# Optimization experiments

Hardware: AMD Instinct MI355X
Metric: run time of the kernel (lower is better)

Reference implementation:

```python
import jax, jax.numpy as jnp
import numpy as np

D = 128      # d_feat / d_model
L = 512      # seq_len
H = 8        # heads (hardcoded in FourierBlock weights)
E = D // H   # head dim = 16
MODES = 64   # low-frequency modes (mode_select='low' -> index = range(MODES))
MA = 25      # moving_avg kernel
NL = 2       # e_layers
DFF = 512
EPS = 1e-5


def _positional(length, dim):
    pos = jnp.arange(length, dtype=jnp.float32)[:, None]
    div = jnp.exp(jnp.arange(0, dim, 2, dtype=jnp.float32) * (-np.log(10000.0) / dim))
    pe = jnp.zeros((length, dim), dtype=jnp.float32)
    pe = pe.at[:, 0::2].set(jnp.sin(pos * div))
    pe = pe.at[:, 1::2].set(jnp.cos(pos * div))
    return pe


def _mov_mean(x, k):
    # series_decomp moving average: replicate-pad (k-1)//2 each side, window mean stride 1
    pad = (k - 1) // 2
    xp = jnp.concatenate([jnp.repeat(x[:, :1], pad, axis=1), x,
                          jnp.repeat(x[:, -1:], pad, axis=1)], axis=1)
    cs = jnp.cumsum(xp, axis=1)
    cs = jnp.concatenate([jnp.zeros_like(cs[:, :1]), cs], axis=1)
    return (cs[:, k:] - cs[:, :-k]) / k


def _fourier_layer(x, Wq, bq, Wo, bo, fwr, fwi):
    # AutoCorrelationLayer(query proj -> FourierBlock -> out proj); k/v projections are unused by FourierBlock
    B = x.shape[0]
    q = (x @ Wq + bq).reshape(B, L, H, E).transpose(0, 2, 3, 1)   # B,H,E,L
    xft = jnp.fft.rfft(q, axis=-1)                                # B,H,E,L//2+1
    Wc = fwr + 1j * fwi                                           # H,E,E,M (complex mode weights)
    sel = jnp.einsum('bhem,heom->bhom', xft[..., :MODES], Wc)
    out_ft = jnp.zeros((B, H, E, L // 2 + 1), dtype=sel.dtype).at[..., :MODES].set(sel)
    y = jnp.fft.irfft(out_ft, n=L, axis=-1)                       # B,H,E,L
    y = y.reshape(B, L, H * E)  # matches torch .view(B, L, -1) on contiguous B,H,E,L
    return y @ Wo + bo


def _enc_layer(x, Wq, bq, Wo, bo, fwr, fwi, W1, W2):
    x = x + _fourier_layer(x, Wq, bq, Wo, bo, fwr, fwi)
    x = x - _mov_mean(x, MA)                                  # decomp1 seasonal part
    y = jax.nn.gelu(x @ W1, approximate=False) @ W2           # 1x1 convs == matmuls, no bias
    s = x + y
    return s - _mov_mean(s, MA)                               # decomp2 seasonal part


def setup_inputs() -> dict:
    key = jax.random.key(0)
    ks = jax.random.split(key, 12)
    B = 128
    scale = 1.0 / (D * D)
    return {
        "x_enc": jax.random.normal(ks[0], (B, D * L), dtype=jnp.float32),
        "x_mark_enc": jax.random.uniform(ks[1], (B, D * L), dtype=jnp.float32),
        "x_dec": jnp.zeros((1,), jnp.float32),
        "x_mark_dec": jnp.zeros((1,), jnp.float32),
        "conv_w": jax.random.normal(ks[2], (D, D, 3), dtype=jnp.float32) * 0.02,
        "Wq": jax.random.normal(ks[3], (NL, D, D), dtype=jnp.float32) * 0.02,
        "bq": jnp.zeros((NL, D), jnp.float32),
        "Wo": jax.random.normal(ks[4], (NL, D, D), dtype=jnp.float32) * 0.02,
        "bo": jnp.zeros((NL, D), jnp.float32),
        "fwr": jax.random.uniform(ks[5], (NL, H, E, E, MODES), dtype=jnp.float32) * scale,
        "fwi": jax.random.uniform(ks[6], (NL, H, E, E, MODES), dtype=jnp.float32) * scale,
        "W1": jax.random.normal(ks[7], (NL, D, DFF), dtype=jnp.float32) * 0.02,
        "W2": jax.random.normal(ks[8], (NL, DFF, D), dtype=jnp.float32) * 0.02,
        "ln_g": jnp.ones((D,), jnp.float32),
        "ln_b": jnp.zeros((D,), jnp.float32),
        "proj_w": jax.random.normal(ks[9], (D * L,), dtype=jnp.float32) * 0.002,
        "proj_b": jnp.zeros((), jnp.float32),
    }


def reference(x_enc, x_mark_enc, x_dec, x_mark_dec, conv_w, Wq, bq, Wo, bo,
              fwr, fwi, W1, W2, ln_g, ln_b, proj_w, proj_b):
    B = x_enc.shape[0]
    x = x_enc.reshape(B, D, L).transpose(0, 2, 1)          # B,L,D
    mark = x_mark_enc.reshape(B, D, L).transpose(0, 2, 1)  # B,L,D
    # TokenEmbedding: Conv1d kernel 3, circular padding, no bias
    xc = x.transpose(0, 2, 1)                              # B,D,L
    xp = jnp.concatenate([xc[:, :, -1:], xc, xc[:, :, :1]], axis=-1)
    tok = jax.lax.conv_general_dilated(xp, conv_w, (1,), 'VALID',
                                       dimension_numbers=('NCH', 'OIH', 'NCH'))
    h = tok.transpose(0, 2, 1) + _positional(L, D)[None]   # + sinusoidal PE (dropout=0)
    for l in range(NL):
        h = _enc_layer(h, Wq[l], bq[l], Wo[l], bo[l], fwr[l], fwi[l], W1[l], W2[l])
    # my_Layernorm: LayerNorm over features, then subtract mean over time axis
    mu = h.mean(-1, keepdims=True)
    var = h.var(-1, keepdims=True)
    hn = (h - mu) / jnp.sqrt(var + EPS) * ln_g + ln_b
    hn = hn - hn.mean(axis=1, keepdims=True)
    o = jax.nn.gelu(hn, approximate=False) * mark          # act + mask-mul
    return o.reshape(B, -1) @ proj_w + proj_b              # (B,) after squeeze
```

## Files before the change

kernel.cpp:

```cpp
#include <hip/hip_runtime.h>
#include <math.h>

#define DFF 512
#define NLAYER 2
#define CS_LD 130
#define SS_LD 130
#define TS2_LD 68

typedef __bf16 bf16x8 __attribute__((ext_vector_type(8)));
typedef __bf16 bf16x4 __attribute__((ext_vector_type(4)));
typedef float f32x4 __attribute__((ext_vector_type(4)));

__device__ __forceinline__ float4 f4_load(const float* p) { return *(const float4*)p; }
__device__ __forceinline__ void f4_store(float* p, float4 v) { *(float4*)p = v; }
__device__ __forceinline__ float4 f4_zero() { return make_float4(0.f, 0.f, 0.f, 0.f); }
__device__ __forceinline__ float gelu_f(float x) {
    return 0.5f * x * (1.0f + erff(x * 0.70710678118654752440f));
}
__device__ __forceinline__ float gelu_fast(float x) {
    float z = 1.5957691216f * (x + 0.044715f * x * x * x);
    float e = __expf(z);
    return x - x / (e + 1.0f);
}
__device__ __forceinline__ void store_bf4(__bf16* p, float4 v) {
    __bf16 t[4] = {(__bf16)v.x, (__bf16)v.y, (__bf16)v.z, (__bf16)v.w};
    *(uint2*)p = *(uint2*)t;
}
__device__ __forceinline__ bf16x8 ld_b64x2(const __bf16* p) {
    bf16x4 lo = *(const bf16x4*)p;
    bf16x4 hi = *(const bf16x4*)(p + 4);
    return __builtin_shufflevector(lo, hi, 0, 1, 2, 3, 4, 5, 6, 7);
}
__device__ __forceinline__ int clampl(int v) { return v < 0 ? 0 : (v > 511 ? 511 : v); }

__global__ __launch_bounds__(256) void k_init(float* __restrict__ pe,
                                              __bf16* __restrict__ Fttb,
                                              __bf16* __restrict__ Gtb) {
    int idx = blockIdx.x * 256 + threadIdx.x;
    {
        int l = idx >> 7, d = idx & 127;
        int j = d >> 1;
        double div = exp((double)(2 * j) * (-log(10000.0) / 128.0));
        double a = (double)l * div;
        pe[idx] = (d & 1) ? (float)cos(a) : (float)sin(a);
    }
    {
        int m2 = idx >> 9, t = idx & 511;
        int m = m2 >> 1;
        int r = (m * t) & 511;
        double ang = (double)r * (6.283185307179586476925287 / 512.0);
        float cv = (float)cos(ang), sv = (float)sin(ang);
        float f = (m2 & 1) ? -sv : cv;
        Fttb[idx] = (__bf16)f;
        float s = (m == 0) ? (1.0f / 512.0f) : (2.0f / 512.0f);
        Gtb[t * 128 + m2] = (__bf16)(f * s);
    }
}

__global__ __launch_bounds__(256) void k_castw(const float* __restrict__ Wq,
                                               const float* __restrict__ Wo,
                                               const float* __restrict__ W1,
                                               const float* __restrict__ W2,
                                               const float* __restrict__ cw,
                                               __bf16* __restrict__ wbf,
                                               __bf16* __restrict__ cwtk) {
    int i = blockIdx.x * 256 + threadIdx.x;
    if (i < 65536) {
        int r = i & 16383, l = (i >> 14) & 1;
        int n = r >> 7, k = r & 127;
        const float* W = (i >= 32768) ? Wo : Wq;
        wbf[i] = (__bf16)W[l * 16384 + k * 128 + n];
    } else if (i < 196608) {
        int j = i - 65536;
        int l = j >> 16, r = j & 65535;
        int f = r >> 7, k = r & 127;
        wbf[i] = (__bf16)W1[l * 65536 + k * 512 + f];
    } else if (i < 327680) {
        int j = i - 196608;
        int l = j >> 16, r = j & 65535;
        int n = r >> 9, f = r & 511;
        wbf[i] = (__bf16)W2[l * 65536 + f * 128 + n];
    } else if (i < 376832) {
        int j = i - 327680;
        int s = j >> 14, r = j & 16383;
        int d = r >> 7, ii = r & 127;
        cwtk[j] = (__bf16)cw[(d * 128 + ii) * 3 + s];
    }
}

__global__ __launch_bounds__(256) void k_xpose(const float* __restrict__ xe,
                                               __bf16* __restrict__ xt) {
    __shared__ float ts[128][65];
    const int b = blockIdx.y, l0 = blockIdx.x * 64;
    for (int idx = threadIdx.x; idx < 128 * 16; idx += 256) {
        int d = idx >> 4, c4 = idx & 15;
        float4 v = f4_load(&xe[((size_t)b * 128 + d) * 512 + l0 + c4 * 4]);
        ts[d][c4 * 4 + 0] = v.x; ts[d][c4 * 4 + 1] = v.y;
        ts[d][c4 * 4 + 2] = v.z; ts[d][c4 * 4 + 3] = v.w;
    }
    __syncthreads();
#pragma unroll
    for (int p = 0; p < 4; ++p) {
        int l = (threadIdx.x >> 4) + p * 16;
        int d0 = (threadIdx.x & 15) * 8;
        __bf16 tmp[8];
#pragma unroll
        for (int j = 0; j < 8; ++j) tmp[j] = (__bf16)ts[d0 + j][l];
        *(uint4*)&xt[((size_t)b * 512 + l0 + l) * 128 + d0] = *(uint4*)tmp;
    }
}

__global__ __launch_bounds__(256, 4) void k_embed_m(const __bf16* __restrict__ xt,
                                                    const __bf16* __restrict__ cwtk,
                                                    const float* __restrict__ pe,
                                                    float* __restrict__ h,
                                                    __bf16* __restrict__ hb) {
    const int b = blockIdx.x >> 3, l0 = (blockIdx.x & 7) * 64;
    const int lane = threadIdx.x & 63, wid = threadIdx.x >> 6;
    const int wrow = (wid & 1) * 32, wcol = (wid >> 1) * 64;
    const int m16 = lane & 15, quad = lane >> 4;
    f32x4 acc[2][4];
#pragma unroll
    for (int a = 0; a < 2; ++a)
#pragma unroll
        for (int bb = 0; bb < 4; ++bb) acc[a][bb] = {0.f, 0.f, 0.f, 0.f};
#pragma unroll
    for (int s = 0; s < 3; ++s) {
#pragma unroll
        for (int ks = 0; ks < 4; ++ks) {
            const int ko = ks * 32 + quad * 8;
            bf16x8 af[2], bfr[4];
#pragma unroll
            for (int rt = 0; rt < 2; ++rt) {
                int gl = (l0 + wrow + rt * 16 + m16 + s - 1) & 511;
                af[rt] = *(const bf16x8*)&xt[(((size_t)b * 512 + gl) << 7) + ko];
            }
#pragma unroll
            for (int ct = 0; ct < 4; ++ct)
                bfr[ct] = *(const bf16x8*)&cwtk[((size_t)(s * 128 + wcol + ct * 16 + m16) << 7) + ko];
#pragma unroll
            for (int rt = 0; rt < 2; ++rt)
#pragma unroll
                for (int ct = 0; ct < 4; ++ct)
                    acc[rt][ct] = __builtin_amdgcn_mfma_f32_16x16x32_bf16(
                        af[rt], bfr[ct], acc[rt][ct], 0, 0, 0);
        }
    }
#pragma unroll
    for (int ct = 0; ct < 4; ++ct) {
        int gcol = wcol + ct * 16 + m16;
#pragma unroll
        for (int rt = 0; rt < 2; ++rt)
#pragma unroll
            for (int r = 0; r < 4; ++r) {
                int l = l0 + wrow + rt * 16 + quad * 4 + r;
                float v = acc[rt][ct][r] + pe[l * 128 + gcol];
                size_t gi = (((size_t)b * 512 + l) << 7) + gcol;
                h[gi] = v;
                hb[gi] = (__bf16)v;
            }
    }
}

__global__ __launch_bounds__(256, 4) void k_qprojT(const __bf16* __restrict__ Xb,
                                                   const __bf16* __restrict__ Wt,
                                                   const float* __restrict__ bias,
                                                   __bf16* __restrict__ qT) {
    const int rowBase = blockIdx.x * 64;
    const int lane = threadIdx.x & 63, wid = threadIdx.x >> 6;
    const int wn = (wid & 1) * 64, wr = (wid >> 1) * 32;
    const int m16 = lane & 15, quad = lane >> 4;
    f32x4 acc[4][2];
#pragma unroll
    for (int a = 0; a < 4; ++a)
#pragma unroll
        for (int b = 0; b < 2; ++b) acc[a][b] = {0.f, 0.f, 0.f, 0.f};
#pragma unroll
    for (int ks = 0; ks < 4; ++ks) {
        const int ko = ks * 32 + quad * 8;
        bf16x8 wf[4], xf[2];
#pragma unroll
        for (int rt = 0; rt < 4; ++rt)
            wf[rt] = *(const bf16x8*)&Wt[((size_t)(wn + rt * 16 + m16) << 7) + ko];
#pragma unroll
        for (int ct = 0; ct < 2; ++ct)
            xf[ct] = *(const bf16x8*)&Xb[((size_t)(rowBase + wr + ct * 16 + m16) << 7) + ko];
#pragma unroll
        for (int rt = 0; rt < 4; ++rt)
#pragma unroll
            for (int ct = 0; ct < 2; ++ct)
                acc[rt][ct] = __builtin_amdgcn_mfma_f32_16x16x32_bf16(
                    wf[rt], xf[ct], acc[rt][ct], 0, 0, 0);
    }
#pragma unroll
    for (int rt = 0; rt < 4; ++rt)
#pragma unroll
        for (int r = 0; r < 4; ++r) {
            int n = wn + rt * 16 + quad * 4 + r;
            float bv = bias[n];
#pragma unroll
            for (int ct = 0; ct < 2; ++ct) {
                int grow = rowBase + wr + ct * 16 + m16;
                qT[(size_t)n * 65536 + grow] = (__bf16)(acc[rt][ct][r] + bv);
            }
        }
}

__global__ __launch_bounds__(128) void k_fdftmix(const __bf16* __restrict__ qT,
                                                 const __bf16* __restrict__ Fttb,
                                                 const float* __restrict__ fwr,
                                                 const float* __restrict__ fwi,
                                                 __bf16* __restrict__ ddb) {
    __shared__ float cs[32][CS_LD];
    const int b = blockIdx.y, d0 = blockIdx.x * 32;
    const int lane = threadIdx.x & 63, wid = threadIdx.x >> 6;
    const int wm = wid * 64;
    const int m16 = lane & 15, quad = lane >> 4;
    f32x4 acc[2][4];
#pragma unroll
    for (int a = 0; a < 2; ++a)
#pragma unroll
        for (int bb = 0; bb < 4; ++bb) acc[a][bb] = {0.f, 0.f, 0.f, 0.f};
    for (int ks = 0; ks < 16; ++ks) {
        const int ko = ks * 32 + quad * 8;
        bf16x8 af[2], bf[4];
#pragma unroll
        for (int rt = 0; rt < 2; ++rt)
            af[rt] = *(const bf16x8*)&qT[(size_t)(d0 + rt * 16 + m16) * 65536 + b * 512 + ko];
#pragma unroll
        for (int ct = 0; ct < 4; ++ct)
            bf[ct] = *(const bf16x8*)&Fttb[(size_t)(wm + ct * 16 + m16) * 512 + ko];
#pragma unroll
        for (int rt = 0; rt < 2; ++rt)
#pragma unroll
            for (int ct = 0; ct < 4; ++ct)
                acc[rt][ct] = __builtin_amdgcn_mfma_f32_16x16x32_bf16(
                    af[rt], bf[ct], acc[rt][ct], 0, 0, 0);
    }
#pragma unroll
    for (int rt = 0; rt < 2; ++rt)
#pragma unroll
        for (int ct = 0; ct < 4; ++ct)
#pragma unroll
            for (int r = 0; r < 4; ++r)
                cs[rt * 16 + quad * 4 + r][wm + ct * 16 + m16] = acc[rt][ct][r];
    __syncthreads();
    const int m = threadIdx.x & 63, og = threadIdx.x >> 6;
#pragma unroll
    for (int lh = 0; lh < 2; ++lh) {
        int hh = (d0 >> 4) + lh;
#pragma unroll
        for (int oi = 0; oi < 8; ++oi) {
            int o = og * 8 + oi;
            float dr = 0.f, di = 0.f;
#pragma unroll
            for (int e = 0; e < 16; ++e) {
                float2 cv = *(const float2*)&cs[lh * 16 + e][2 * m];
                float wr = fwr[(((size_t)hh * 16 + e) * 16 + o) * 64 + m];
                float wi = fwi[(((size_t)hh * 16 + e) * 16 + o) * 64 + m];
                dr += cv.x * wr - cv.y * wi;
                di += cv.x * wi + cv.y * wr;
            }
            __bf16 t2[2] = {(__bf16)dr, (__bf16)di};
            *(uint*)&ddb[((size_t)b * 128 + hh * 16 + o) * 128 + 2 * m] = *(uint*)t2;
        }
    }
}

__global__ __launch_bounds__(256, 4) void k_idft_m(const __bf16* __restrict__ ddb,
                                                   const __bf16* __restrict__ Gtb,
                                                   __bf16* __restrict__ y) {
    const int b = blockIdx.y;
    const int t0 = (blockIdx.x & 3) * 128, hob = (blockIdx.x >> 2) * 64;
    const int lane = threadIdx.x & 63, wid = threadIdx.x >> 6;
    const int wt = (wid & 1) * 64, wh = (wid >> 1) * 32;
    const int m16 = lane & 15, quad = lane >> 4;
    f32x4 acc[4][2];
#pragma unroll
    for (int a = 0; a < 4; ++a)
#pragma unroll
        for (int bb = 0; bb < 2; ++bb) acc[a][bb] = {0.f, 0.f, 0.f, 0.f};
#pragma unroll
    for (int ks = 0; ks < 4; ++ks) {
        const int ko = ks * 32 + quad * 8;
        bf16x8 af[4], bf[2];
#pragma unroll
        for (int rt = 0; rt < 4; ++rt)
            af[rt] = *(const bf16x8*)&Gtb[(size_t)(t0 + wt + rt * 16 + m16) * 128 + ko];
#pragma unroll
        for (int ct = 0; ct < 2; ++ct)
            bf[ct] = *(const bf16x8*)&ddb[((size_t)b * 128 + hob + wh + ct * 16 + m16) * 128 + ko];
#pragma unroll
        for (int rt = 0; rt < 4; ++rt)
#pragma unroll
            for (int ct = 0; ct < 2; ++ct)
                acc[rt][ct] = __builtin_amdgcn_mfma_f32_16x16x32_bf16(
                    af[rt], bf[ct], acc[rt][ct], 0, 0, 0);
    }
#pragma unroll
    for (int rt = 0; rt < 4; ++rt)
#pragma unroll
        for (int ct = 0; ct < 2; ++ct) {
            int ho = hob + wh + ct * 16 + m16;
            int tb = t0 + wt + rt * 16 + quad * 4;
            __bf16 tmp[4] = {(__bf16)acc[rt][ct][0], (__bf16)acc[rt][ct][1],
                             (__bf16)acc[rt][ct][2], (__bf16)acc[rt][ct][3]};
            *(uint2*)&y[((size_t)b * 128 + ho) * 512 + tb] = *(uint2*)tmp;
        }
}

__global__ __launch_bounds__(256, 3) void k_mgd(const __bf16* __restrict__ yb,
                                                const __bf16* __restrict__ Wt,
                                                const float* __restrict__ bias,
                                                const float* __restrict__ hres,
                                                float* __restrict__ outf,
                                                __bf16* __restrict__ outb) {
    __shared__ float ss[96 * SS_LD];
    const int b = blockIdx.x >> 3, l0 = (blockIdx.x & 7) * 64;
    const int lane = threadIdx.x & 63, wid = threadIdx.x >> 6;
    const int wrow = (wid & 1) * 48, wcol = (wid >> 1) * 64;
    const int m16 = lane & 15, quad = lane >> 4;
    f32x4 acc[3][4];
#pragma unroll
    for (int a = 0; a < 3; ++a)
#pragma unroll
        for (int bb = 0; bb < 4; ++bb) acc[a][bb] = {0.f, 0.f, 0.f, 0.f};
#pragma unroll
    for (int ks = 0; ks < 4; ++ks) {
        const int ko = ks * 32 + quad * 8;
        bf16x8 af[3], bfr[4];
#pragma unroll
        for (int rt = 0; rt < 3; ++rt) {
            int gl = clampl(l0 - 16 + wrow + rt * 16 + m16);
            af[rt] = *(const bf16x8*)&yb[(((size_t)b * 512 + gl) << 7) + ko];
        }
#pragma unroll
        for (int ct = 0; ct < 4; ++ct)
            bfr[ct] = *(const bf16x8*)&Wt[((size_t)(wcol + ct * 16 + m16) << 7) + ko];
#pragma unroll
        for (int rt = 0; rt < 3; ++rt)
#pragma unroll
            for (int ct = 0; ct < 4; ++ct)
                acc[rt][ct] = __builtin_amdgcn_mfma_f32_16x16x32_bf16(
                    af[rt], bfr[ct], acc[rt][ct], 0, 0, 0);
    }
#pragma unroll
    for (int ct = 0; ct < 4; ++ct) {
        int col = wcol + ct * 16 + m16;
        float bv = bias[col];
#pragma unroll
        for (int rt = 0; rt < 3; ++rt)
#pragma unroll
            for (int r = 0; r < 4; ++r) {
                int row = wrow + rt * 16 + quad * 4 + r;
                int gl = clampl(l0 - 16 + row);
                ss[row * SS_LD + col] =
                    acc[rt][ct][r] + bv + hres[(((size_t)b * 512 + gl) << 7) + col];
            }
    }
    __syncthreads();
    const int dg = threadIdx.x & 31, lg = threadIdx.x >> 5;
    const int d0 = dg * 4, base = lg * 8;
    float4 s = f4_zero();
#pragma unroll
    for (int w = 0; w < 25; ++w) {
        float4 v = f4_load(&ss[(base + 4 + w) * SS_LD + d0]);
        s.x += v.x; s.y += v.y; s.z += v.z; s.w += v.w;
    }
    const float inv = 1.0f / 25.0f;
#pragma unroll
    for (int i = 0; i < 8; ++i) {
        float4 x = f4_load(&ss[(base + 16 + i) * SS_LD + d0]);
        float4 o = make_float4(x.x - s.x * inv, x.y - s.y * inv,
                               x.z - s.z * inv, x.w - s.w * inv);
        size_t gi = (((size_t)b * 512 + l0 + base + i) << 7) + d0;
        f4_store(&outf[gi], o);
        store_bf4(&outb[gi], o);
        if (i < 7) {
            float4 a = f4_load(&ss[(base + 29 + i) * SS_LD + d0]);
            float4 r = f4_load(&ss[(base + 4 + i) * SS_LD + d0]);
            s.x += a.x - r.x; s.y += a.y - r.y; s.z += a.z - r.z; s.w += a.w - r.w;
        }
    }
}

__global__ __launch_bounds__(256, 3) void k_ffd(const __bf16* __restrict__ Xb,
                                                const float* __restrict__ Xf,
                                                const __bf16* __restrict__ W1t,
                                                const __bf16* __restrict__ W2t,
                                                float* __restrict__ outf,
                                                __bf16* __restrict__ outb) {
    __shared__ __align__(16) float ss[96 * SS_LD];
    __bf16* ts = (__bf16*)ss;
    const int b = blockIdx.x >> 3, l0 = (blockIdx.x & 7) * 64;
    const int lane = threadIdx.x & 63, wid = threadIdx.x >> 6;
    const int wrow = (wid & 1) * 48;
    const int wcolF = (wid >> 1) * 32;
    const int wcolO = (wid >> 1) * 64;
    const int m16 = lane & 15, quad = lane >> 4;
    f32x4 acc2[3][4];
#pragma unroll
    for (int a = 0; a < 3; ++a)
#pragma unroll
        for (int bb = 0; bb < 4; ++bb) acc2[a][bb] = {0.f, 0.f, 0.f, 0.f};

    for (int fc = 0; fc < 8; ++fc) {
        const int f0 = fc * 64;
        f32x4 c1[3][2];
#pragma unroll
        for (int a = 0; a < 3; ++a)
#pragma unroll
            for (int bb = 0; bb < 2; ++bb) c1[a][bb] = {0.f, 0.f, 0.f, 0.f};
#pragma unroll
        for (int ks = 0; ks < 4; ++ks) {
            const int ko = ks * 32 + quad * 8;
            bf16x8 af[3], bfr[2];
#pragma unroll
            for (int rt = 0; rt < 3; ++rt) {
                int gl = clampl(l0 - 16 + wrow + rt * 16 + m16);
                af[rt] = *(const bf16x8*)&Xb[(((size_t)b * 512 + gl) << 7) + ko];
            }
#pragma unroll
            for (int ct = 0; ct < 2; ++ct)
                bfr[ct] = *(const bf16x8*)&W1t[((size_t)(f0 + wcolF + ct * 16 + m16) << 7) + ko];
#pragma unroll
            for (int rt = 0; rt < 3; ++rt)
#pragma unroll
                for (int ct = 0; ct < 2; ++ct)
                    c1[rt][ct] = __builtin_amdgcn_mfma_f32_16x16x32_bf16(
                        af[rt], bfr[ct], c1[rt][ct], 0, 0, 0);
        }
#pragma unroll
        for (int rt = 0; rt < 3; ++rt)
#pragma unroll
            for (int ct = 0; ct < 2; ++ct)
#pragma unroll
                for (int r = 0; r < 4; ++r) {
                    int lrow = wrow + rt * 16 + quad * 4 + r;
                    int lcol = wcolF + ct * 16 + m16;
                    ts[lrow * TS2_LD + lcol] = (__bf16)gelu_fast(c1[rt][ct][r]);
                }
        __syncthreads();
#pragma unroll
        for (int ks2 = 0; ks2 < 2; ++ks2) {
            const int ko2 = ks2 * 32 + quad * 8;
            bf16x8 af[3], bfr[4];
#pragma unroll
            for (int rt = 0; rt < 3; ++rt)
                af[rt] = ld_b64x2(&ts[(wrow + rt * 16 + m16) * TS2_LD + ko2]);
#pragma unroll
            for (int ct = 0; ct < 4; ++ct)
                bfr[ct] = *(const bf16x8*)&W2t[((size_t)(wcolO + ct * 16 + m16) << 9) + f0 + ko2];
#pragma unroll
            for (int rt = 0; rt < 3; ++rt)
#pragma unroll
                for (int ct = 0; ct < 4; ++ct)
                    acc2[rt][ct] = __builtin_amdgcn_mfma_f32_16x16x32_bf16(
                        af[rt], bfr[ct], acc2[rt][ct], 0, 0, 0);
        }
        __syncthreads();
    }
#pragma unroll
    for (int ct = 0; ct < 4; ++ct) {
        int col = wcolO + ct * 16 + m16;
#pragma unroll
        for (int rt = 0; rt < 3; ++rt)
#pragma unroll
            for (int r = 0; r < 4; ++r) {
                int row = wrow + rt * 16 + quad * 4 + r;
                int gl = clampl(l0 - 16 + row);
                ss[row * SS_LD + col] =
                    acc2[rt][ct][r] + Xf[(((size_t)b * 512 + gl) << 7) + col];
            }
    }
    __syncthreads();
    const int dg = threadIdx.x & 31, lg = threadIdx.x >> 5;
    const int d0 = dg * 4, base = lg * 8;
    float4 s = f4_zero();
#pragma unroll
    for (int w = 0; w < 25; ++w) {
        float4 v = f4_load(&ss[(base + 4 + w) * SS_LD + d0]);
        s.x += v.x; s.y += v.y; s.z += v.z; s.w += v.w;
    }
    const float inv = 1.0f / 25.0f;
#pragma unroll
    for (int i = 0; i < 8; ++i) {
        float4 x = f4_load(&ss[(base + 16 + i) * SS_LD + d0]);
        float4 o = make_float4(x.x - s.x * inv, x.y - s.y * inv,
                               x.z - s.z * inv, x.w - s.w * inv);
        size_t gi = (((size_t)b * 512 + l0 + base + i) << 7) + d0;
        f4_store(&outf[gi], o);
        store_bf4(&outb[gi], o);
        if (i < 7) {
            float4 a = f4_load(&ss[(base + 29 + i) * SS_LD + d0]);
            float4 r = f4_load(&ss[(base + 4 + i) * SS_LD + d0]);
            s.x += a.x - r.x; s.y += a.y - r.y; s.z += a.z - r.z; s.w += a.w - r.w;
        }
    }
}

__global__ __launch_bounds__(256) void k_ln(const float* __restrict__ X,
                                            const float* __restrict__ g,
                                            const float* __restrict__ bb,
                                            float* __restrict__ out) {
    const int row = blockIdx.x * 4 + (threadIdx.x >> 6);
    const int lane = threadIdx.x & 63;
    float2 v = *(const float2*)&X[(size_t)row * 128 + lane * 2];
    float s = v.x + v.y, ss = v.x * v.x + v.y * v.y;
#pragma unroll
    for (int o = 32; o; o >>= 1) {
        s += __shfl_xor(s, o);
        ss += __shfl_xor(ss, o);
    }
    float mu = s * (1.0f / 128.0f);
    float var = ss * (1.0f / 128.0f) - mu * mu;
    float rstd = rsqrtf(var + 1e-5f);
    float2 gg = *(const float2*)&g[lane * 2];
    float2 bv = *(const float2*)&bb[lane * 2];
    float2 o;
    o.x = (v.x - mu) * rstd * gg.x + bv.x;
    o.y = (v.y - mu) * rstd * gg.y + bv.y;
    *(float2*)&out[(size_t)row * 128 + lane * 2] = o;
}

__global__ __launch_bounds__(128) void k_colmean(const float* __restrict__ X,
                                                 float* __restrict__ cm) {
    const int b = blockIdx.y, l0 = blockIdx.x * 64, d = threadIdx.x;
    float s = 0.f;
    for (int l = l0; l < l0 + 64; ++l) s += X[((size_t)b * 512 + l) * 128 + d];
    atomicAdd(&cm[b * 128 + d], s);
}

__global__ __launch_bounds__(128) void k_final(const float* __restrict__ hn,
                                               const float* __restrict__ cm,
                                               const float* __restrict__ mark,
                                               const float* __restrict__ pw,
                                               const float* __restrict__ pb,
                                               float* __restrict__ out) {
    const int b = blockIdx.y, l0 = blockIdx.x * 128, d = threadIdx.x;
    const float c = cm[b * 128 + d] * (1.0f / 512.0f);
    float acc = 0.f;
    for (int l = l0; l < l0 + 128; ++l) {
        float v = hn[((size_t)b * 512 + l) * 128 + d] - c;
        acc += gelu_f(v) * mark[((size_t)b * 128 + d) * 512 + l] * pw[l * 128 + d];
    }
    __shared__ float red[2];
#pragma unroll
    for (int o = 32; o; o >>= 1) acc += __shfl_xor(acc, o);
    if ((threadIdx.x & 63) == 0) red[threadIdx.x >> 6] = acc;
    __syncthreads();
    if (threadIdx.x == 0) {
        float tot = red[0] + red[1];
        if (blockIdx.x == 0) tot += pb[0];
        atomicAdd(&out[b], tot);
    }
}

extern "C" void kernel_launch(void* const* d_in, const int* in_sizes, int n_in,
                              void* d_out, int out_size, void* d_ws, size_t ws_size,
                              hipStream_t stream) {
    const float* xe   = (const float*)d_in[0];
    const float* mark = (const float*)d_in[1];
    const float* cw   = (const float*)d_in[4];
    const float* Wq   = (const float*)d_in[5];
    const float* bq   = (const float*)d_in[6];
    const float* Wo   = (const float*)d_in[7];
    const float* bo   = (const float*)d_in[8];
    const float* fwr  = (const float*)d_in[9];
    const float* fwi  = (const float*)d_in[10];
    const float* W1   = (const float*)d_in[11];
    const float* W2   = (const float*)d_in[12];
    const float* lng  = (const float*)d_in[13];
    const float* lnb  = (const float*)d_in[14];
    const float* pw   = (const float*)d_in[15];
    const float* pb   = (const float*)d_in[16];
    float* out = (float*)d_out;

    float* ws    = (float*)d_ws;
    __bf16* Fttb = (__bf16*)ws;
    __bf16* Gtb  = (__bf16*)(ws + 65536);
    float* h     = ws + 131072;
    float* bufA  = ws + 8519680;
    __bf16* hb0  = (__bf16*)(ws + 16908288);
    __bf16* hb1  = (__bf16*)(ws + 21102592);
    float* yrg   = ws + 25296896;
    float* cm    = ws + 29491200;
    __bf16* wbf  = (__bf16*)(ws + 29507584);
    float* pe    = yrg;
    __bf16* cwtk = (__bf16*)(yrg + 65536);
    __bf16* yb   = (__bf16*)yrg;
    __bf16* xt   = (__bf16*)bufA;
    __bf16* qT   = (__bf16*)bufA;
    __bf16* ddb  = (__bf16*)(bufA + 4194304);
    __bf16* Wqt  = wbf;
    __bf16* Wot  = wbf + 32768;
    __bf16* W1t  = wbf + 65536;
    __bf16* W2t  = wbf + 196608;

    k_init<<<256, 256, 0, stream>>>(pe, Fttb, Gtb);
    k_castw<<<1472, 256, 0, stream>>>(Wq, Wo, W1, W2, cw, wbf, cwtk);
    k_xpose<<<dim3(8, 128), 256, 0, stream>>>(xe, xt);
    k_embed_m<<<1024, 256, 0, stream>>>(xt, cwtk, pe, h, hb0);
    for (int l = 0; l < NLAYER; ++l) {
        k_qprojT<<<1024, 256, 0, stream>>>(hb0, Wqt + l * 16384, bq + l * 128, qT);
        k_fdftmix<<<dim3(4, 128), 128, 0, stream>>>(qT, Fttb, fwr + l * 131072,
                                                    fwi + l * 131072, ddb);
        k_idft_m<<<dim3(8, 128), 256, 0, stream>>>(ddb, Gtb, yb);
        k_mgd<<<1024, 256, 0, stream>>>(yb, Wot + l * 16384, bo + l * 128,
                                        h, bufA, hb1);
        k_ffd<<<1024, 256, 0, stream>>>(hb1, bufA, W1t + l * 65536,
                                        W2t + l * 65536, h, hb0);
    }
    k_ln<<<16384, 256, 0, stream>>>(h, lng, lnb, bufA);
    hipMemsetAsync(cm, 0, 16384 * sizeof(float), stream);
    k_colmean<<<dim3(8, 128), 128, 0, stream>>>(bufA, cm);
    hipMemsetAsync(d_out, 0, 128 * sizeof(float), stream);
    k_final<<<dim3(4, 128), 128, 0, stream>>>(bufA, cm, mark, pw, pb, out);

    (void)in_sizes; (void)n_in; (void)out_size; (void)ws_size;
}
```

Baseline: 675.4 us.

## Stage activation tiles in swizzled LDS and double-buffer FFN intermediate; widen fdftmix blocks

k_mgd and k_ffd now copy the 96-row activation tile into XOR-swizzled shared memory once, and the MFMA loops read A-fragments from there instead of global memory. k_ffd also double-buffers its GELU intermediate tile, so one barrier per chunk can be dropped. k_fdftmix goes from 128 to 256 threads, with each wave taking one 16-row slab, which gives more waves per block. In exchange, k_ffd uses more shared memory, which may lower occupancy, and both kernels pay for an upfront staging step plus extra barriers.

```diff
diff --git a/kernel.cpp b/kernel.cpp
--- a/kernel.cpp
+++ b/kernel.cpp
@@ -206,7 +206,7 @@
         }
 }
 
-__global__ __launch_bounds__(128) void k_fdftmix(const __bf16* __restrict__ qT,
+__global__ __launch_bounds__(256) void k_fdftmix(const __bf16* __restrict__ qT,
                                                  const __bf16* __restrict__ Fttb,
                                                  const float* __restrict__ fwr,
                                                  const float* __restrict__ fwi,
@@ -214,44 +214,36 @@
     __shared__ float cs[32][CS_LD];
     const int b = blockIdx.y, d0 = blockIdx.x * 32;
     const int lane = threadIdx.x & 63, wid = threadIdx.x >> 6;
-    const int wm = wid * 64;
+    const int wd = (wid & 1) * 16;
+    const int wm = (wid >> 1) * 64;
     const int m16 = lane & 15, quad = lane >> 4;
-    f32x4 acc[2][4];
-#pragma unroll
-    for (int a = 0; a < 2; ++a)
-#pragma unroll
-        for (int bb = 0; bb < 4; ++bb) acc[a][bb] = {0.f, 0.f, 0.f, 0.f};
+    f32x4 acc[4];
+#pragma unroll
+    for (int ct = 0; ct < 4; ++ct) acc[ct] = {0.f, 0.f, 0.f, 0.f};
     for (int ks = 0; ks < 16; ++ks) {
         const int ko = ks * 32 + quad * 8;
-        bf16x8 af[2], bf[4];
-#pragma unroll
-        for (int rt = 0; rt < 2; ++rt)
-            af[rt] = *(const bf16x8*)&qT[(size_t)(d0 + rt * 16 + m16) * 65536 + b * 512 + ko];
+        bf16x8 af = *(const bf16x8*)&qT[(size_t)(d0 + wd + m16) * 65536 + b * 512 + ko];
+        bf16x8 bf[4];
 #pragma unroll
         for (int ct = 0; ct < 4; ++ct)
             bf[ct] = *(const bf16x8*)&Fttb[(size_t)(wm + ct * 16 + m16) * 512 + ko];
 #pragma unroll
-        for (int rt = 0; rt < 2; ++rt)
-#pragma unroll
-            for (int ct = 0; ct < 4; ++ct)
-                acc[rt][ct] = __builtin_amdgcn_mfma_f32_16x16x32_bf16(
-                    af[rt], bf[ct], acc[rt][ct], 0, 0, 0);
-    }
-#pragma unroll
-    for (int rt = 0; rt < 2; ++rt)
-#pragma unroll
         for (int ct = 0; ct < 4; ++ct)
-#pragma unroll
-            for (int r = 0; r < 4; ++r)
-                cs[rt * 16 + quad * 4 + r][wm + ct * 16 + m16] = acc[rt][ct][r];
+            acc[ct] = __builtin_amdgcn_mfma_f32_16x16x32_bf16(af, bf[ct], acc[ct], 0, 0, 0);
+    }
+#pragma unroll
+    for (int ct = 0; ct < 4; ++ct)
+#pragma unroll
+        for (int r = 0; r < 4; ++r)
+            cs[wd + quad * 4 + r][wm + ct * 16 + m16] = acc[ct][r];
     __syncthreads();
     const int m = threadIdx.x & 63, og = threadIdx.x >> 6;
 #pragma unroll
     for (int lh = 0; lh < 2; ++lh) {
         int hh = (d0 >> 4) + lh;
 #pragma unroll
-        for (int oi = 0; oi < 8; ++oi) {
-            int o = og * 8 + oi;
+        for (int oi = 0; oi < 4; ++oi) {
+            int o = og * 4 + oi;
             float dr = 0.f, di = 0.f;
 #pragma unroll
             for (int e = 0; e < 16; ++e) {
@@ -315,8 +307,17 @@
                                                 const float* __restrict__ hres,
                                                 float* __restrict__ outf,
                                                 __bf16* __restrict__ outb) {
-    __shared__ float ss[96 * SS_LD];
+    __shared__ __align__(16) float ss[96 * SS_LD];
+    __bf16* xs = (__bf16*)ss;
     const int b = blockIdx.x >> 3, l0 = (blockIdx.x & 7) * 64;
+    for (int it = 0; it < 6; ++it) {
+        int c = it * 256 + threadIdx.x;
+        int r = c >> 4, g = c & 15;
+        int gl = clampl(l0 - 16 + r);
+        *(uint4*)&xs[(r << 7) + ((g ^ (r & 7)) << 3)] =
+            *(const uint4*)&yb[(((size_t)b * 512 + gl) << 7) + (g << 3)];
+    }
+    __syncthreads();
     const int lane = threadIdx.x & 63, wid = threadIdx.x >> 6;
     const int wrow = (wid & 1) * 48, wcol = (wid >> 1) * 64;
     const int m16 = lane & 15, quad = lane >> 4;
@@ -331,8 +332,8 @@
         bf16x8 af[3], bfr[4];
 #pragma unroll
         for (int rt = 0; rt < 3; ++rt) {
-            int gl = clampl(l0 - 16 + wrow + rt * 16 + m16);
-            af[rt] = *(const bf16x8*)&yb[(((size_t)b * 512 + gl) << 7) + ko];
+            int row = wrow + rt * 16 + m16;
+            af[rt] = *(const bf16x8*)&xs[(row << 7) + (((ks * 4 + quad) ^ (row & 7)) << 3)];
         }
 #pragma unroll
         for (int ct = 0; ct < 4; ++ct)
@@ -344,6 +345,7 @@
                 acc[rt][ct] = __builtin_amdgcn_mfma_f32_16x16x32_bf16(
                     af[rt], bfr[ct], acc[rt][ct], 0, 0, 0);
     }
+    __syncthreads();
 #pragma unroll
     for (int ct = 0; ct < 4; ++ct) {
         int col = wcol + ct * 16 + m16;
@@ -390,9 +392,18 @@
                                                 const __bf16* __restrict__ W2t,
                                                 float* __restrict__ outf,
                                                 __bf16* __restrict__ outb) {
-    __shared__ __align__(16) float ss[96 * SS_LD];
-    __bf16* ts = (__bf16*)ss;
+    __shared__ __align__(16) unsigned char smem[50688];
+    float* ss = (float*)smem;
+    __bf16* xs = (__bf16*)smem;
     const int b = blockIdx.x >> 3, l0 = (blockIdx.x & 7) * 64;
+    for (int it = 0; it < 6; ++it) {
+        int c = it * 256 + threadIdx.x;
+        int r = c >> 4, g = c & 15;
+        int gl = clampl(l0 - 16 + r);
+        *(uint4*)&xs[(r << 7) + ((g ^ (r & 7)) << 3)] =
+            *(const uint4*)&Xb[(((size_t)b * 512 + gl) << 7) + (g << 3)];
+    }
+    __syncthreads();
     const int lane = threadIdx.x & 63, wid = threadIdx.x >> 6;
     const int wrow = (wid & 1) * 48;
     const int wcolF = (wid >> 1) * 32;
@@ -405,6 +416,7 @@
         for (int bb = 0; bb < 4; ++bb) acc2[a][bb] = {0.f, 0.f, 0.f, 0.f};
 
     for (int fc = 0; fc < 8; ++fc) {
+        __bf16* ts = (__bf16*)(smem + 24576 + (fc & 1) * 13056);
         const int f0 = fc * 64;
         f32x4 c1[3][2];
 #pragma unroll
@@ -417,8 +429,8 @@
             bf16x8 af[3], bfr[2];
 #pragma unroll
             for (int rt = 0; rt < 3; ++rt) {
-                int gl = clampl(l0 - 16 + wrow + rt * 16 + m16);
-                af[rt] = *(const bf16x8*)&Xb[(((size_t)b * 512 + gl) << 7) + ko];
+                int row = wrow + rt * 16 + m16;
+                af[rt] = *(const bf16x8*)&xs[(row << 7) + (((ks * 4 + quad) ^ (row & 7)) << 3)];
             }
 #pragma unroll
             for (int ct = 0; ct < 2; ++ct)
@@ -458,8 +470,8 @@
                     acc2[rt][ct] = __builtin_amdgcn_mfma_f32_16x16x32_bf16(
                         af[rt], bfr[ct], acc2[rt][ct], 0, 0, 0);
         }
-        __syncthreads();
-    }
+    }
+    __syncthreads();
 #pragma unroll
     for (int ct = 0; ct < 4; ++ct) {
         int col = wcolO + ct * 16 + m16;
@@ -603,7 +615,7 @@
     k_embed_m<<<1024, 256, 0, stream>>>(xt, cwtk, pe, h, hb0);
     for (int l = 0; l < NLAYER; ++l) {
         k_qprojT<<<1024, 256, 0, stream>>>(hb0, Wqt + l * 16384, bq + l * 128, qT);
-        k_fdftmix<<<dim3(4, 128), 128, 0, stream>>>(qT, Fttb, fwr + l * 131072,
+        k_fdftmix<<<dim3(4, 128), 256, 0, stream>>>(qT, Fttb, fwr + l * 131072,
                                                     fwi + l * 131072, ddb);
         k_idft_m<<<dim3(8, 128), 256, 0, stream>>>(ddb, Gtb, yb);
         k_mgd<<<1024, 256, 0, stream>>>(yb, Wot + l * 16384, bo + l * 128,
```

New measurement: 620.5 us. -8.1%, faster.
